# Performance work log

Hardware: AMD Instinct MI355X
Metric: run time of the kernel (lower is better)

## Reference

```python
import jax, jax.numpy as jnp
import numpy as np

B, N, E, H = 16, 577, 1024, 16          # batch, tokens (1 cls + 24x24 patches), embed, heads
HD = E // H
LORA_E, LORA_R = 4, 16                   # LoRA experts, rank
AD_E, AD_D = 4, 64                       # adapter experts, bottleneck
FF = 4 * E


def setup_inputs() -> dict:
    key = jax.random.key(0)
    ks = jax.random.split(key, 12)
    p = lambda i, shape: jax.random.normal(ks[i], shape, dtype=jnp.float32) * 0.02
    return {
        "tokens": jax.random.normal(ks[0], (B, N, E), dtype=jnp.float32),
        "ln1_g": jnp.ones((E,), jnp.float32), "ln1_b": jnp.zeros((E,), jnp.float32),
        "qkv_w": p(1, (3 * E, E)), "qkv_b": jnp.zeros((3 * E,), jnp.float32),
        "proj_w": p(2, (E, E)), "proj_b": jnp.zeros((E,), jnp.float32),
        "lora_gate_w": p(3, (LORA_E, E)),
        "lora_A": p(4, (LORA_E, LORA_R, E)),
        "lora_B": p(5, (LORA_E, 3 * E, LORA_R)),
        "ln2_g": jnp.ones((E,), jnp.float32), "ln2_b": jnp.zeros((E,), jnp.float32),
        "fc1_w": p(6, (FF, E)), "fc1_b": jnp.zeros((FF,), jnp.float32),
        "fc2_w": p(7, (E, FF)), "fc2_b": jnp.zeros((E,), jnp.float32),
        "ad_gate_w": p(8, (AD_E, E)),
        "ad_down_w": p(9, (AD_E, AD_D, E)), "ad_down_b": jnp.zeros((AD_E, AD_D), jnp.float32),
        "ad_up_w": p(10, (AD_E, E, AD_D)), "ad_up_b": jnp.zeros((AD_E, E), jnp.float32),
    }


def _ln(x, g, b):
    m = x.mean(-1, keepdims=True)
    v = ((x - m) ** 2).mean(-1, keepdims=True)
    return (x - m) * jax.lax.rsqrt(v + 1e-6) * g + b


def reference(tokens, ln1_g, ln1_b, qkv_w, qkv_b, proj_w, proj_b,
              lora_gate_w, lora_A, lora_B, ln2_g, ln2_b,
              fc1_w, fc1_b, fc2_w, fc2_b,
              ad_gate_w, ad_down_w, ad_down_b, ad_up_w, ad_up_b):
    # ---- attention with MoE-LoRA delta on fused QKV ----
    normed = _ln(tokens, ln1_g, ln1_b)                      # [B,N,E]
    qkv = normed @ qkv_w.T + qkv_b                          # [B,N,3E]
    gates = jax.nn.softmax(normed @ lora_gate_w.T, axis=-1)  # [B,N,X]
    h = jnp.einsum('bnd,xrd->bnxr', normed, lora_A)         # low-rank down
    delta = jnp.einsum('bnxr,bnx,xor->bno', h, gates, lora_B)  # gate-weighted up
    qkv = (qkv + delta).reshape(B, N, 3, H, HD).transpose(2, 0, 3, 1, 4)
    q, k, v = qkv[0], qkv[1], qkv[2]                        # [B,H,N,hd]
    scores = jnp.einsum('bhqd,bhkd->bhqk', q, k) * (HD ** -0.5)
    probs = jax.nn.softmax(scores, axis=-1)
    ctx = jnp.einsum('bhqk,bhkd->bhqd', probs, v)
    ctx = ctx.transpose(0, 2, 1, 3).reshape(B, N, E)
    tokens = tokens + (ctx @ proj_w.T + proj_b)
    # ---- MLP + MoE adapter branch (shared norm2 input) ----
    mlp_in = _ln(tokens, ln2_g, ln2_b)
    mlp_out = jax.nn.gelu(mlp_in @ fc1_w.T + fc1_b, approximate=False) @ fc2_w.T + fc2_b
    ag = jax.nn.softmax(mlp_in @ ad_gate_w.T, axis=-1)       # [B,N,Xa]
    ah = jax.nn.gelu(jnp.einsum('bnd,xhd->bnxh', mlp_in, ad_down_w) + ad_down_b,
                     approximate=False)
    ad_out = (jnp.einsum('bnxh,bnx,xoh->bno', ah, ag, ad_up_w)
              + jnp.einsum('bnx,xo->bno', ag, ad_up_b))
    return tokens + mlp_out + ad_out
```

## Files before the change

kernel.cpp:

```cpp
#include <hip/hip_runtime.h>
#include <math.h>

#define TOK 9232
#define EMB 1024
#define NQKV 3072
#define FFD 4096
#define NSEQ 577

typedef __bf16 bf16x8 __attribute__((ext_vector_type(8)));
typedef float f32x4 __attribute__((ext_vector_type(4)));
typedef unsigned short ushort8 __attribute__((ext_vector_type(8)));
typedef unsigned short ushort4v __attribute__((ext_vector_type(4)));

typedef __attribute__((address_space(3))) unsigned int lds_u32_t;
typedef const __attribute__((address_space(1))) unsigned int glob_u32_t;

__device__ __forceinline__ void async16(void* lds, const void* g) {
    __builtin_amdgcn_global_load_lds((glob_u32_t*)g, (lds_u32_t*)lds, 16, 0, 0);
}

__device__ __forceinline__ unsigned short f2bf(float f) {
    unsigned int u = __builtin_bit_cast(unsigned int, f);
    u = (u + 0x7fffu + ((u >> 16) & 1u)) >> 16;
    return (unsigned short)u;
}
__device__ __forceinline__ float bf2f(unsigned short s) {
    unsigned int u = ((unsigned int)s) << 16;
    return __builtin_bit_cast(float, u);
}
__device__ __forceinline__ float gelu_exact(float x) {
    return 0.5f * x * (1.0f + erff(x * 0.70710678118654752f));
}

__global__ void k_pack_all(const float* __restrict__ s_qkv, const float* __restrict__ s_proj,
                           const float* __restrict__ s_fc1, const float* __restrict__ s_fc2,
                           const float* __restrict__ s_la,  const float* __restrict__ s_ad,
                           unsigned short* __restrict__ d_qkv, unsigned short* __restrict__ d_proj,
                           unsigned short* __restrict__ d_fc1, unsigned short* __restrict__ d_fc2,
                           unsigned short* __restrict__ d_la,  unsigned short* __restrict__ d_ad) {
    int stride = gridDim.x * 256;
    for (int i4 = blockIdx.x * 256 + threadIdx.x; i4 < 3227648; i4 += stride) {
        const float* s; unsigned short* d; int local;
        if (i4 < 786432)       { s = s_qkv;  d = d_qkv;  local = i4; }
        else if (i4 < 1048576) { s = s_proj; d = d_proj; local = i4 - 786432; }
        else if (i4 < 2097152) { s = s_fc1;  d = d_fc1;  local = i4 - 1048576; }
        else if (i4 < 3145728) { s = s_fc2;  d = d_fc2;  local = i4 - 2097152; }
        else if (i4 < 3162112) { s = s_la;   d = d_la;   local = i4 - 3145728; }
        else                   { s = s_ad;   d = d_ad;   local = i4 - 3162112; }
        float4 v = ((const float4*)s)[local];
        ushort4v o;
        o[0] = f2bf(v.x); o[1] = f2bf(v.y); o[2] = f2bf(v.z); o[3] = f2bf(v.w);
        ((ushort4v*)d)[local] = o;
    }
}
__global__ void k_pack_bcat(const float* __restrict__ Bw, unsigned short* __restrict__ out) {
    int i = blockIdx.x * 256 + threadIdx.x;
    if (i >= 3072 * 64) return;
    int o = i >> 6, j = i & 63, x = j >> 4, r = j & 15;
    out[o * 64 + j] = f2bf(Bw[x * 3072 * 16 + o * 16 + r]);
}
__global__ void k_pack_u(const float* __restrict__ Uw, unsigned short* __restrict__ out) {
    int i = blockIdx.x * 256 + threadIdx.x;
    if (i >= 1024 * 256) return;
    int o = i >> 8, j = i & 255, x = j >> 6, h = j & 63;
    out[o * 256 + j] = f2bf(Uw[x * 65536 + o * 64 + h]);
}

__global__ __launch_bounds__(256) void k_ln_gates(const float* __restrict__ x,
                                                  const float* __restrict__ g,
                                                  const float* __restrict__ b,
                                                  const float* __restrict__ gw,
                                                  unsigned short* __restrict__ out,
                                                  float* __restrict__ gates) {
    int t = blockIdx.x;
    int tid = threadIdx.x;
    const float* xp = x + (size_t)t * EMB;
    float4 v = ((const float4*)xp)[tid];
    float s = v.x + v.y + v.z + v.w;
    float sq = v.x * v.x + v.y * v.y + v.z * v.z + v.w * v.w;
    #pragma unroll
    for (int off = 32; off > 0; off >>= 1) {
        s += __shfl_down(s, off);
        sq += __shfl_down(sq, off);
    }
    __shared__ float red[8];
    if ((tid & 63) == 0) { red[tid >> 6] = s; red[(tid >> 6) + 4] = sq; }
    __syncthreads();
    float S = red[0] + red[1] + red[2] + red[3];
    float SQ = red[4] + red[5] + red[6] + red[7];
    float mean = S * (1.0f / EMB);
    float var = SQ * (1.0f / EMB) - mean * mean;
    float rstd = rsqrtf(var + 1e-6f);
    float4 gv = ((const float4*)g)[tid];
    float4 bv = ((const float4*)b)[tid];
    float n0 = (v.x - mean) * rstd * gv.x + bv.x;
    float n1 = (v.y - mean) * rstd * gv.y + bv.y;
    float n2 = (v.z - mean) * rstd * gv.z + bv.z;
    float n3 = (v.w - mean) * rstd * gv.w + bv.w;
    ushort4v o;
    o[0] = f2bf(n0); o[1] = f2bf(n1); o[2] = f2bf(n2); o[3] = f2bf(n3);
    ((ushort4v*)(out + (size_t)t * EMB))[tid] = o;
    float p[4];
    #pragma unroll
    for (int xx = 0; xx < 4; ++xx) {
        float4 gr = ((const float4*)(gw + xx * EMB))[tid];
        p[xx] = n0 * gr.x + n1 * gr.y + n2 * gr.z + n3 * gr.w;
    }
    #pragma unroll
    for (int off = 32; off > 0; off >>= 1) {
        #pragma unroll
        for (int xx = 0; xx < 4; ++xx) p[xx] += __shfl_down(p[xx], off);
    }
    __shared__ float red2[4][4];
    if ((tid & 63) == 0) {
        #pragma unroll
        for (int xx = 0; xx < 4; ++xx) red2[tid >> 6][xx] = p[xx];
    }
    __syncthreads();
    if (tid == 0) {
        float l[4];
        #pragma unroll
        for (int xx = 0; xx < 4; ++xx) l[xx] = red2[0][xx] + red2[1][xx] + red2[2][xx] + red2[3][xx];
        float m = fmaxf(fmaxf(l[0], l[1]), fmaxf(l[2], l[3]));
        float e[4], ssum = 0.f;
        #pragma unroll
        for (int xx = 0; xx < 4; ++xx) { e[xx] = expf(l[xx] - m); ssum += e[xx]; }
        float inv = 1.0f / ssum;
        #pragma unroll
        for (int xx = 0; xx < 4; ++xx) gates[t * 4 + xx] = e[xx] * inv;
    }
}

__global__ __launch_bounds__(256) void k_fc2init(const float* __restrict__ tok2,
                                                 const float* __restrict__ fc2b,
                                                 const float* __restrict__ ag,
                                                 const float* __restrict__ upb,
                                                 float* __restrict__ out) {
    int t = blockIdx.x;
    int tid = threadIdx.x;
    float g0 = ag[t * 4 + 0], g1 = ag[t * 4 + 1], g2 = ag[t * 4 + 2], g3 = ag[t * 4 + 3];
    float4 b0 = ((const float4*)(upb + 0 * EMB))[tid];
    float4 b1 = ((const float4*)(upb + 1 * EMB))[tid];
    float4 b2 = ((const float4*)(upb + 2 * EMB))[tid];
    float4 b3 = ((const float4*)(upb + 3 * EMB))[tid];
    float4 fb = ((const float4*)fc2b)[tid];
    float4 r = ((const float4*)(tok2 + (size_t)t * EMB))[tid];
    r.x += fb.x + g0 * b0.x + g1 * b1.x + g2 * b2.x + g3 * b3.x;
    r.y += fb.y + g0 * b0.y + g1 * b1.y + g2 * b2.y + g3 * b3.y;
    r.z += fb.z + g0 * b0.z + g1 * b1.z + g2 * b2.z + g3 * b3.z;
    r.w += fb.w + g0 * b0.w + g1 * b1.w + g2 * b2.w + g3 * b3.w;
    ((float4*)(out + (size_t)t * EMB))[tid] = r;
}

#define VMCNT8 asm volatile("s_waitcnt vmcnt(8)" ::: "memory")
#define BAR __builtin_amdgcn_s_barrier()

template<bool GELU, bool BF16OUT, int GG>
__global__ __launch_bounds__(256) void k_gemm(
    const unsigned short* __restrict__ A, int lda,
    const unsigned short* __restrict__ W, int ldw, int K1,
    int M, int N,
    const unsigned short* __restrict__ A2, const unsigned short* __restrict__ W2, int K2,
    const float* __restrict__ bias, const float* __restrict__ resid,
    const float* __restrict__ aux,
    void* __restrict__ Cout, int ldc, int gy)
{
    __shared__ unsigned short As[3][128][32];
    __shared__ unsigned short Ws[3][128][32];
    int tid = threadIdx.x;
    int nwg = gridDim.x, orig = blockIdx.x;
    int xcd = orig & 7, lid = orig >> 3;
    int q = nwg >> 3, r = nwg & 7;
    int wg = (xcd < r ? xcd * (q + 1) : r * (q + 1) + (xcd - r) * q) + lid;
    int bm128 = (wg / gy) * 128;
    int bn128 = (wg % gy) * 128;

    int l = tid & 63, w = tid >> 6;
    int wr = w >> 1, wc = w & 1;
    int lr = l & 15, lk = (l >> 4) * 8;
    int srow = l >> 2;
    int sslot = (l & 3) * 8;

    int KT1 = K1 >> 5, KT2 = K2 >> 5;
    int KT = KT1 + KT2;

    int ra0 = bm128 + w * 32 + srow;      if (ra0 > M - 1) ra0 = M - 1;
    int ra1 = bm128 + w * 32 + 16 + srow; if (ra1 > M - 1) ra1 = M - 1;
    int rb0 = bn128 + w * 32 + srow;      if (rb0 > N - 1) rb0 = N - 1;
    int rb1 = bn128 + w * 32 + 16 + srow; if (rb1 > N - 1) rb1 = N - 1;
    const unsigned short* pA0 = A + (size_t)ra0 * lda + sslot;
    const unsigned short* pA1 = A + (size_t)ra1 * lda + sslot;
    const unsigned short* pB0 = W + (size_t)rb0 * ldw + sslot;
    const unsigned short* pB1 = W + (size_t)rb1 * ldw + sslot;
    const unsigned short* A2s = A2 ? A2 : A;
    const unsigned short* W2s = W2 ? W2 : W;
    int K2s = A2 ? K2 : lda;
    const unsigned short* qA0 = A2s + (size_t)ra0 * K2s + sslot;
    const unsigned short* qA1 = A2s + (size_t)ra1 * K2s + sslot;
    const unsigned short* qB0 = W2s + (size_t)rb0 * K2s + sslot;
    const unsigned short* qB1 = W2s + (size_t)rb1 * K2s + sslot;

    f32x4 acc[4][4];
    #pragma unroll
    for (int m = 0; m < 4; ++m)
        #pragma unroll
        for (int n = 0; n < 4; ++n) acc[m][n] = (f32x4){0.f, 0.f, 0.f, 0.f};

#define STAGE(s_, sb_) do {                                          \
    char* da_ = (char*)As + (sb_) * 8192 + w * 2048;                 \
    char* db_ = (char*)Ws + (sb_) * 8192 + w * 2048;                 \
    int ss_ = (s_);                                                  \
    if (ss_ < KT1) {                                                 \
        int ko_ = ss_ << 5;                                          \
        async16(da_,        pA0 + ko_);                              \
        async16(da_ + 1024, pA1 + ko_);                              \
        async16(db_,        pB0 + ko_);                              \
        async16(db_ + 1024, pB1 + ko_);                              \
    } else {                                                         \
        int ko_ = (ss_ - KT1) << 5;                                  \
        async16(da_,        qA0 + ko_);                              \
        async16(da_ + 1024, qA1 + ko_);                              \
        async16(db_,        qB0 + ko_);                              \
        async16(db_ + 1024, qB1 + ko_);                              \
    }                                                                \
} while (0)

    STAGE(0, 0);
    STAGE(1, 1);

    int cb = 0, sb = 2;
    #pragma unroll 1
    for (int t = 0; t < KT; ++t) {
        int s = t + 2; if (s >= KT) s = 0;
        STAGE(s, sb);
        VMCNT8;
        BAR;
        bf16x8 af[4], bfr[4];
        #pragma unroll
        for (int m = 0; m < 4; ++m) af[m] = *(const bf16x8*)&As[cb][wr * 64 + m * 16 + lr][lk];
        #pragma unroll
        for (int n = 0; n < 4; ++n) bfr[n] = *(const bf16x8*)&Ws[cb][wc * 64 + n * 16 + lr][lk];
        __builtin_amdgcn_s_setprio(1);
        #pragma unroll
        for (int m = 0; m < 4; ++m)
            #pragma unroll
            for (int n = 0; n < 4; ++n)
                acc[m][n] = __builtin_amdgcn_mfma_f32_16x16x32_bf16(af[m], bfr[n], acc[m][n], 0, 0, 0);
        __builtin_amdgcn_s_setprio(0);
        BAR;
        cb = (cb == 2) ? 0 : cb + 1;
        sb = (sb == 2) ? 0 : sb + 1;
    }
#undef STAGE

    int rbase = bm128 + wr * 64;
    int cbase = bn128 + wc * 64;
    #pragma unroll
    for (int n = 0; n < 4; ++n) {
        int col = cbase + n * 16 + lr;
        if (col >= N) continue;
        float bv = bias ? bias[col] : 0.0f;
        #pragma unroll
        for (int m = 0; m < 4; ++m) {
            #pragma unroll
            for (int rr = 0; rr < 4; ++rr) {
                int row = rbase + m * 16 + (l >> 4) * 4 + rr;
                if (row >= M) continue;
                float c = acc[m][n][rr] + bv;
                if (GELU) c = gelu_exact(c);
                if (GG > 0) c *= aux[row * 4 + col / (GG > 0 ? GG : 1)];
                if (resid) c += resid[(size_t)row * ldc + col];
                if (BF16OUT) ((unsigned short*)Cout)[(size_t)row * ldc + col] = f2bf(c);
                else ((float*)Cout)[(size_t)row * ldc + col] = c;
            }
        }
    }
}

__global__ __launch_bounds__(256) void k_attn(const unsigned short* __restrict__ qkv,
                                              unsigned short* __restrict__ ctx) {
    int bh = blockIdx.x;
    int qt = blockIdx.y;
    int b = bh >> 4, h = bh & 15;
    int tid = threadIdx.x;
    int l = tid & 63;
    int w = tid >> 6;
    int lr = l & 15;
    int lk = (l >> 4) * 8;

    __shared__ unsigned short Qs[64][72];
    __shared__ unsigned short Ks[64][72];
    __shared__ unsigned short Vt[64][72];
    __shared__ unsigned short Ps[64][72];

    const size_t base = (size_t)b * NSEQ * NQKV + (size_t)h * 64;
    int q0 = qt * 64;

    {
        int row = tid >> 2, ds = (tid & 3) * 16;
        int qrow = q0 + row;
        if (qrow < NSEQ) {
            const unsigned short* src = qkv + base + (size_t)qrow * NQKV + ds;
            #pragma unroll
            for (int j = 0; j < 16; ++j) Qs[row][ds + j] = f2bf(bf2f(src[j]) * 0.125f);
        } else {
            #pragma unroll
            for (int j = 0; j < 16; ++j) Qs[row][ds + j] = 0;
        }
    }

    float m_run[4], l_run[4];
    f32x4 o[4];
    #pragma unroll
    for (int r = 0; r < 4; ++r) { m_run[r] = -1e30f; l_run[r] = 0.0f; }
    #pragma unroll
    for (int n = 0; n < 4; ++n) o[n] = (f32x4){0.f, 0.f, 0.f, 0.f};

    for (int kt = 0; kt < 10; ++kt) {
        __syncthreads();
        {
            int row = tid >> 2, ds = (tid & 3) * 16;
            int key = kt * 64 + row;
            if (key < NSEQ) {
                const unsigned short* ksrc = qkv + base + (size_t)key * NQKV + 1024 + ds;
                *(ushort8*)&Ks[row][ds] = *(const ushort8*)ksrc;
                *(ushort8*)&Ks[row][ds + 8] = *(const ushort8*)(ksrc + 8);
                const unsigned short* vsrc = qkv + base + (size_t)key * NQKV + 2048 + ds;
                #pragma unroll
                for (int j = 0; j < 16; ++j) Vt[ds + j][row] = vsrc[j];
            } else {
                ushort8 z = {};
                *(ushort8*)&Ks[row][ds] = z;
                *(ushort8*)&Ks[row][ds + 8] = z;
                #pragma unroll
                for (int j = 0; j < 16; ++j) Vt[ds + j][row] = 0;
            }
        }
        __syncthreads();

        f32x4 s[4];
        #pragma unroll
        for (int n = 0; n < 4; ++n) s[n] = (f32x4){0.f, 0.f, 0.f, 0.f};
        #pragma unroll
        for (int ks = 0; ks < 2; ++ks) {
            bf16x8 qa = *(const bf16x8*)&Qs[w * 16 + lr][ks * 32 + lk];
            #pragma unroll
            for (int n = 0; n < 4; ++n) {
                bf16x8 kb = *(const bf16x8*)&Ks[n * 16 + lr][ks * 32 + lk];
                s[n] = __builtin_amdgcn_mfma_f32_16x16x32_bf16(qa, kb, s[n], 0, 0, 0);
            }
        }
        #pragma unroll
        for (int n = 0; n < 4; ++n) {
            int col = kt * 64 + n * 16 + lr;
            if (col >= NSEQ) {
                #pragma unroll
                for (int r = 0; r < 4; ++r) s[n][r] = -1e30f;
            }
        }
        float tmax[4];
        #pragma unroll
        for (int r = 0; r < 4; ++r)
            tmax[r] = fmaxf(fmaxf(s[0][r], s[1][r]), fmaxf(s[2][r], s[3][r]));
        #pragma unroll
        for (int off = 1; off < 16; off <<= 1) {
            #pragma unroll
            for (int r = 0; r < 4; ++r) tmax[r] = fmaxf(tmax[r], __shfl_xor(tmax[r], off));
        }
        float alpha[4], rs[4];
        #pragma unroll
        for (int r = 0; r < 4; ++r) {
            float mn = fmaxf(m_run[r], tmax[r]);
            alpha[r] = __expf(m_run[r] - mn);
            m_run[r] = mn;
            rs[r] = 0.0f;
        }
        #pragma unroll
        for (int n = 0; n < 4; ++n) {
            #pragma unroll
            for (int r = 0; r < 4; ++r) {
                float p = __expf(s[n][r] - m_run[r]);
                s[n][r] = p;
                rs[r] += p;
            }
        }
        #pragma unroll
        for (int off = 1; off < 16; off <<= 1) {
            #pragma unroll
            for (int r = 0; r < 4; ++r) rs[r] += __shfl_xor(rs[r], off);
        }
        #pragma unroll
        for (int r = 0; r < 4; ++r) l_run[r] = l_run[r] * alpha[r] + rs[r];
        #pragma unroll
        for (int n = 0; n < 4; ++n) {
            #pragma unroll
            for (int r = 0; r < 4; ++r) o[n][r] *= alpha[r];
        }
        #pragma unroll
        for (int n = 0; n < 4; ++n) {
            #pragma unroll
            for (int r = 0; r < 4; ++r)
                Ps[w * 16 + (l >> 4) * 4 + r][n * 16 + lr] = f2bf(s[n][r]);
        }
        __syncthreads();
        #pragma unroll
        for (int ks = 0; ks < 2; ++ks) {
            bf16x8 pa = *(const bf16x8*)&Ps[w * 16 + lr][ks * 32 + lk];
            #pragma unroll
            for (int n = 0; n < 4; ++n) {
                bf16x8 vb = *(const bf16x8*)&Vt[n * 16 + lr][ks * 32 + lk];
                o[n] = __builtin_amdgcn_mfma_f32_16x16x32_bf16(pa, vb, o[n], 0, 0, 0);
            }
        }
    }
    #pragma unroll
    for (int r = 0; r < 4; ++r) {
        int qrow = q0 + w * 16 + (l >> 4) * 4 + r;
        if (qrow < NSEQ) {
            float inv = (l_run[r] > 0.f) ? 1.0f / l_run[r] : 0.0f;
            #pragma unroll
            for (int n = 0; n < 4; ++n)
                ctx[((size_t)b * NSEQ + qrow) * EMB + h * 64 + n * 16 + lr] = f2bf(o[n][r] * inv);
        }
    }
}

extern "C" void kernel_launch(void* const* d_in, const int* in_sizes, int n_in,
                              void* d_out, int out_size, void* d_ws, size_t ws_size,
                              hipStream_t stream) {
    const float* tokens      = (const float*)d_in[0];
    const float* ln1_g       = (const float*)d_in[1];
    const float* ln1_b       = (const float*)d_in[2];
    const float* qkv_w       = (const float*)d_in[3];
    const float* qkv_b       = (const float*)d_in[4];
    const float* proj_w      = (const float*)d_in[5];
    const float* proj_b      = (const float*)d_in[6];
    const float* lora_gate_w = (const float*)d_in[7];
    const float* lora_A      = (const float*)d_in[8];
    const float* lora_B      = (const float*)d_in[9];
    const float* ln2_g       = (const float*)d_in[10];
    const float* ln2_b       = (const float*)d_in[11];
    const float* fc1_w       = (const float*)d_in[12];
    const float* fc1_b       = (const float*)d_in[13];
    const float* fc2_w       = (const float*)d_in[14];
    const float* fc2_b       = (const float*)d_in[15];
    const float* ad_gate_w   = (const float*)d_in[16];
    const float* ad_down_w   = (const float*)d_in[17];
    const float* ad_down_b   = (const float*)d_in[18];
    const float* ad_up_w     = (const float*)d_in[19];
    const float* ad_up_b     = (const float*)d_in[20];

    char* ws = (char*)d_ws;
    size_t off = 0;
    auto alloc = [&](size_t bytes) -> void* {
        void* p = ws + off;
        off += (bytes + 255) & ~(size_t)255;
        return p;
    };

    unsigned short* w_qkv  = (unsigned short*)alloc((size_t)NQKV * EMB * 2);
    unsigned short* w_proj = (unsigned short*)alloc((size_t)EMB * EMB * 2);
    unsigned short* w_fc1  = (unsigned short*)alloc((size_t)FFD * EMB * 2);
    unsigned short* w_fc2  = (unsigned short*)alloc((size_t)EMB * FFD * 2);
    unsigned short* w_acat = (unsigned short*)alloc((size_t)64 * EMB * 2);
    unsigned short* w_bcat = (unsigned short*)alloc((size_t)NQKV * 64 * 2);
    unsigned short* w_dcat = (unsigned short*)alloc((size_t)256 * EMB * 2);
    unsigned short* w_u    = (unsigned short*)alloc((size_t)EMB * 256 * 2);

    unsigned short* u1 = (unsigned short*)alloc((size_t)TOK * EMB * 2);
    unsigned short* u2 = (unsigned short*)alloc((size_t)TOK * EMB * 2);
    unsigned short* u3 = (unsigned short*)alloc((size_t)TOK * FFD * 2);
    float* tok2  = (float*)alloc((size_t)TOK * EMB * 4);
    unsigned short* hw  = (unsigned short*)alloc((size_t)TOK * 64 * 2);
    unsigned short* ahw = (unsigned short*)alloc((size_t)TOK * 256 * 2);
    float* gates = (float*)alloc((size_t)TOK * 4 * 4);
    float* ag    = (float*)alloc((size_t)TOK * 4 * 4);

    unsigned short* normed = u1;
    unsigned short* mlpin  = u1;
    unsigned short* ctx    = u2;
    unsigned short* qkv    = u3;
    unsigned short* h1     = u3;

    k_pack_all<<<2048, 256, 0, stream>>>(qkv_w, proj_w, fc1_w, fc2_w, lora_A, ad_down_w,
                                         w_qkv, w_proj, w_fc1, w_fc2, w_acat, w_dcat);
    k_pack_bcat<<<(NQKV * 64 + 255) / 256, 256, 0, stream>>>(lora_B, w_bcat);
    k_pack_u<<<(EMB * 256 + 255) / 256, 256, 0, stream>>>(ad_up_w, w_u);

    k_ln_gates<<<TOK, 256, 0, stream>>>(tokens, ln1_g, ln1_b, lora_gate_w, normed, gates);
    k_gemm<false, true, 16><<<73, 256, 0, stream>>>(
        normed, EMB, w_acat, EMB, EMB, TOK, 64,
        nullptr, nullptr, 0, nullptr, nullptr, gates, hw, 64, 1);
    k_gemm<false, true, 0><<<73 * 24, 256, 0, stream>>>(
        normed, EMB, w_qkv, EMB, EMB, TOK, NQKV,
        hw, w_bcat, 64, qkv_b, nullptr, nullptr, qkv, NQKV, 24);
    k_attn<<<dim3(256, 10), 256, 0, stream>>>(qkv, ctx);
    k_gemm<false, false, 0><<<73 * 8, 256, 0, stream>>>(
        ctx, EMB, w_proj, EMB, EMB, TOK, EMB,
        nullptr, nullptr, 0, proj_b, tokens, nullptr, tok2, EMB, 8);
    k_ln_gates<<<TOK, 256, 0, stream>>>(tok2, ln2_g, ln2_b, ad_gate_w, mlpin, ag);
    k_gemm<true, true, 64><<<73 * 2, 256, 0, stream>>>(
        mlpin, EMB, w_dcat, EMB, EMB, TOK, 256,
        nullptr, nullptr, 0, ad_down_b, nullptr, ag, ahw, 256, 2);
    k_fc2init<<<TOK, 256, 0, stream>>>(tok2, fc2_b, ag, ad_up_b, (float*)d_out);
    k_gemm<true, true, 0><<<73 * 32, 256, 0, stream>>>(
        mlpin, EMB, w_fc1, EMB, EMB, TOK, FFD,
        nullptr, nullptr, 0, fc1_b, nullptr, nullptr, h1, FFD, 32);
    k_gemm<false, false, 0><<<73 * 8, 256, 0, stream>>>(
        h1, FFD, w_fc2, FFD, FFD, TOK, EMB,
        ahw, w_u, 256, nullptr, (const float*)d_out, nullptr, (float*)d_out, EMB, 8);
}
```

Measured before the change: 739.4 us.

## Template GEMM M-tile size, swizzle LDS, and drop one barrier per k-step

Makes the GEMM's M-tile height a template parameter, so the narrow-N GEMMs (proj, fc2, LoRA-A, adapter-down) use 64-row tiles and launch roughly twice as many workgroups to fill the CUs. The LDS layout gets an XOR swizzle on the k-slot to cut bank conflicts on the fragment reads. The k-loop now waits for outstanding loads and barriers before issuing the next stage, which removes the trailing barrier. The trade-off is less data reuse per 64-row tile and a tighter prefetch distance.

```diff
diff --git a/kernel.cpp b/kernel.cpp
--- a/kernel.cpp
+++ b/kernel.cpp
@@ -152,10 +152,9 @@
     ((float4*)(out + (size_t)t * EMB))[tid] = r;
 }
 
-#define VMCNT8 asm volatile("s_waitcnt vmcnt(8)" ::: "memory")
 #define BAR __builtin_amdgcn_s_barrier()
 
-template<bool GELU, bool BF16OUT, int GG>
+template<bool GELU, bool BF16OUT, int GG, int MF>
 __global__ __launch_bounds__(256) void k_gemm(
     const unsigned short* __restrict__ A, int lda,
     const unsigned short* __restrict__ W, int ldw, int K1,
@@ -165,103 +164,113 @@
     const float* __restrict__ aux,
     void* __restrict__ Cout, int ldc, int gy)
 {
-    __shared__ unsigned short As[3][128][32];
-    __shared__ unsigned short Ws[3][128][32];
+    constexpr int CA = MF * 2;
+    constexpr int CPW = (CA + 8) / 4;
+    constexpr int BUFB = (CA + 8) * 1024;
+    __shared__ __attribute__((aligned(16))) char Sbuf[3 * BUFB];
+
     int tid = threadIdx.x;
     int nwg = gridDim.x, orig = blockIdx.x;
     int xcd = orig & 7, lid = orig >> 3;
     int q = nwg >> 3, r = nwg & 7;
     int wg = (xcd < r ? xcd * (q + 1) : r * (q + 1) + (xcd - r) * q) + lid;
-    int bm128 = (wg / gy) * 128;
-    int bn128 = (wg % gy) * 128;
+    int bm = (wg / gy) * (MF * 32);
+    int bn = (wg % gy) * 128;
 
     int l = tid & 63, w = tid >> 6;
     int wr = w >> 1, wc = w & 1;
-    int lr = l & 15, lk = (l >> 4) * 8;
-    int srow = l >> 2;
-    int sslot = (l & 3) * 8;
+    int lr = l & 15;
+    int sslot = (((l & 3) ^ ((l >> 3) & 3)) << 3);
 
     int KT1 = K1 >> 5, KT2 = K2 >> 5;
     int KT = KT1 + KT2;
 
-    int ra0 = bm128 + w * 32 + srow;      if (ra0 > M - 1) ra0 = M - 1;
-    int ra1 = bm128 + w * 32 + 16 + srow; if (ra1 > M - 1) ra1 = M - 1;
-    int rb0 = bn128 + w * 32 + srow;      if (rb0 > N - 1) rb0 = N - 1;
-    int rb1 = bn128 + w * 32 + 16 + srow; if (rb1 > N - 1) rb1 = N - 1;
-    const unsigned short* pA0 = A + (size_t)ra0 * lda + sslot;
-    const unsigned short* pA1 = A + (size_t)ra1 * lda + sslot;
-    const unsigned short* pB0 = W + (size_t)rb0 * ldw + sslot;
-    const unsigned short* pB1 = W + (size_t)rb1 * ldw + sslot;
     const unsigned short* A2s = A2 ? A2 : A;
     const unsigned short* W2s = W2 ? W2 : W;
     int K2s = A2 ? K2 : lda;
-    const unsigned short* qA0 = A2s + (size_t)ra0 * K2s + sslot;
-    const unsigned short* qA1 = A2s + (size_t)ra1 * K2s + sslot;
-    const unsigned short* qB0 = W2s + (size_t)rb0 * K2s + sslot;
-    const unsigned short* qB1 = W2s + (size_t)rb1 * K2s + sslot;
-
-    f32x4 acc[4][4];
-    #pragma unroll
-    for (int m = 0; m < 4; ++m)
+
+    const unsigned short* sp1[CPW];
+    const unsigned short* sp2[CPW];
+    int ldsu[CPW];
+    #pragma unroll
+    for (int j = 0; j < CPW; ++j) {
+        int c = w * CPW + j;
+        ldsu[j] = c << 10;
+        if (c < CA) {
+            int rw = bm + c * 16 + (l >> 2); if (rw > M - 1) rw = M - 1;
+            sp1[j] = A + (size_t)rw * lda + sslot;
+            sp2[j] = A2s + (size_t)rw * K2s + sslot;
+        } else {
+            int rw = bn + (c - CA) * 16 + (l >> 2); if (rw > N - 1) rw = N - 1;
+            sp1[j] = W + (size_t)rw * ldw + sslot;
+            sp2[j] = W2s + (size_t)rw * K2s + sslot;
+        }
+    }
+
+    int psl = ((l >> 4) ^ ((lr >> 1) & 3)) << 4;
+    int offA[MF], offB[4];
+    #pragma unroll
+    for (int m = 0; m < MF; ++m) offA[m] = ((wr * (MF * 16) + m * 16 + lr) << 6) + psl;
+    #pragma unroll
+    for (int n = 0; n < 4; ++n) offB[n] = (CA << 10) + ((wc * 64 + n * 16 + lr) << 6) + psl;
+
+    f32x4 acc[MF][4];
+    #pragma unroll
+    for (int m = 0; m < MF; ++m)
         #pragma unroll
         for (int n = 0; n < 4; ++n) acc[m][n] = (f32x4){0.f, 0.f, 0.f, 0.f};
 
-#define STAGE(s_, sb_) do {                                          \
-    char* da_ = (char*)As + (sb_) * 8192 + w * 2048;                 \
-    char* db_ = (char*)Ws + (sb_) * 8192 + w * 2048;                 \
-    int ss_ = (s_);                                                  \
-    if (ss_ < KT1) {                                                 \
-        int ko_ = ss_ << 5;                                          \
-        async16(da_,        pA0 + ko_);                              \
-        async16(da_ + 1024, pA1 + ko_);                              \
-        async16(db_,        pB0 + ko_);                              \
-        async16(db_ + 1024, pB1 + ko_);                              \
-    } else {                                                         \
-        int ko_ = (ss_ - KT1) << 5;                                  \
-        async16(da_,        qA0 + ko_);                              \
-        async16(da_ + 1024, qA1 + ko_);                              \
-        async16(db_,        qB0 + ko_);                              \
-        async16(db_ + 1024, qB1 + ko_);                              \
-    }                                                                \
-} while (0)
-
-    STAGE(0, 0);
-    STAGE(1, 1);
+    auto stage = [&](int ss, int sb_) {
+        char* db = Sbuf + sb_ * BUFB;
+        if (ss < KT1) {
+            int ko = ss << 5;
+            #pragma unroll
+            for (int j = 0; j < CPW; ++j) async16(db + ldsu[j], sp1[j] + ko);
+        } else {
+            int ko = (ss - KT1) << 5;
+            #pragma unroll
+            for (int j = 0; j < CPW; ++j) async16(db + ldsu[j], sp2[j] + ko);
+        }
+    };
+
+    stage(0, 0);
+    stage(1, 1);
 
     int cb = 0, sb = 2;
     #pragma unroll 1
     for (int t = 0; t < KT; ++t) {
+        if constexpr (CPW == 4) asm volatile("s_waitcnt vmcnt(4)" ::: "memory");
+        else                    asm volatile("s_waitcnt vmcnt(3)" ::: "memory");
+        BAR;
+        __builtin_amdgcn_sched_barrier(0);
         int s = t + 2; if (s >= KT) s = 0;
-        STAGE(s, sb);
-        VMCNT8;
-        BAR;
-        bf16x8 af[4], bfr[4];
-        #pragma unroll
-        for (int m = 0; m < 4; ++m) af[m] = *(const bf16x8*)&As[cb][wr * 64 + m * 16 + lr][lk];
-        #pragma unroll
-        for (int n = 0; n < 4; ++n) bfr[n] = *(const bf16x8*)&Ws[cb][wc * 64 + n * 16 + lr][lk];
+        stage(s, sb);
+        const char* base = Sbuf + cb * BUFB;
+        bf16x8 af[MF], bfr[4];
+        #pragma unroll
+        for (int m = 0; m < MF; ++m) af[m] = *(const bf16x8*)(base + offA[m]);
+        #pragma unroll
+        for (int n = 0; n < 4; ++n) bfr[n] = *(const bf16x8*)(base + offB[n]);
         __builtin_amdgcn_s_setprio(1);
         #pragma unroll
-        for (int m = 0; m < 4; ++m)
+        for (int m = 0; m < MF; ++m)
             #pragma unroll
             for (int n = 0; n < 4; ++n)
                 acc[m][n] = __builtin_amdgcn_mfma_f32_16x16x32_bf16(af[m], bfr[n], acc[m][n], 0, 0, 0);
         __builtin_amdgcn_s_setprio(0);
-        BAR;
         cb = (cb == 2) ? 0 : cb + 1;
         sb = (sb == 2) ? 0 : sb + 1;
     }
-#undef STAGE
-
-    int rbase = bm128 + wr * 64;
-    int cbase = bn128 + wc * 64;
+
+    int rbase = bm + wr * (MF * 16);
+    int cbase = bn + wc * 64;
     #pragma unroll
     for (int n = 0; n < 4; ++n) {
         int col = cbase + n * 16 + lr;
         if (col >= N) continue;
         float bv = bias ? bias[col] : 0.0f;
         #pragma unroll
-        for (int m = 0; m < 4; ++m) {
+        for (int m = 0; m < MF; ++m) {
             #pragma unroll
             for (int rr = 0; rr < 4; ++rr) {
                 int row = rbase + m * 16 + (l >> 4) * 4 + rr;
@@ -488,25 +497,25 @@
     k_pack_u<<<(EMB * 256 + 255) / 256, 256, 0, stream>>>(ad_up_w, w_u);
 
     k_ln_gates<<<TOK, 256, 0, stream>>>(tokens, ln1_g, ln1_b, lora_gate_w, normed, gates);
-    k_gemm<false, true, 16><<<73, 256, 0, stream>>>(
+    k_gemm<false, true, 16, 2><<<145, 256, 0, stream>>>(
         normed, EMB, w_acat, EMB, EMB, TOK, 64,
         nullptr, nullptr, 0, nullptr, nullptr, gates, hw, 64, 1);
-    k_gemm<false, true, 0><<<73 * 24, 256, 0, stream>>>(
+    k_gemm<false, true, 0, 4><<<73 * 24, 256, 0, stream>>>(
         normed, EMB, w_qkv, EMB, EMB, TOK, NQKV,
         hw, w_bcat, 64, qkv_b, nullptr, nullptr, qkv, NQKV, 24);
     k_attn<<<dim3(256, 10), 256, 0, stream>>>(qkv, ctx);
-    k_gemm<false, false, 0><<<73 * 8, 256, 0, stream>>>(
+    k_gemm<false, false, 0, 2><<<145 * 8, 256, 0, stream>>>(
         ctx, EMB, w_proj, EMB, EMB, TOK, EMB,
         nullptr, nullptr, 0, proj_b, tokens, nullptr, tok2, EMB, 8);
     k_ln_gates<<<TOK, 256, 0, stream>>>(tok2, ln2_g, ln2_b, ad_gate_w, mlpin, ag);
-    k_gemm<true, true, 64><<<73 * 2, 256, 0, stream>>>(
+    k_gemm<true, true, 64, 2><<<145 * 2, 256, 0, stream>>>(
         mlpin, EMB, w_dcat, EMB, EMB, TOK, 256,
         nullptr, nullptr, 0, ad_down_b, nullptr, ag, ahw, 256, 2);
     k_fc2init<<<TOK, 256, 0, stream>>>(tok2, fc2_b, ag, ad_up_b, (float*)d_out);
-    k_gemm<true, true, 0><<<73 * 32, 256, 0, stream>>>(
+    k_gemm<true, true, 0, 4><<<73 * 32, 256, 0, stream>>>(
         mlpin, EMB, w_fc1, EMB, EMB, TOK, FFD,
         nullptr, nullptr, 0, fc1_b, nullptr, nullptr, h1, FFD, 32);
-    k_gemm<false, false, 0><<<73 * 8, 256, 0, stream>>>(
+    k_gemm<false, false, 0, 2><<<145 * 8, 256, 0, stream>>>(
         h1, FFD, w_fc2, FFD, FFD, TOK, EMB,
         ahw, w_u, 256, nullptr, (const float*)d_out, nullptr, (float*)d_out, EMB, 8);
 }
```

Result: faster. 721.6 us (-2.4%).
